# Kernel optimization log

Measured on AMD Instinct MI355X. Metric: run time of the kernel, lower is better.

The kernel has to match this reference:

```python
import jax, jax.numpy as jnp
import numpy as np
import math

IN_CH = 256
EMBED = 128


def setup_inputs() -> dict:
    key = jax.random.key(0)
    k1, k2, k3, k4, k5 = jax.random.split(key, 5)
    N, C, H, W = 4, IN_CH, 64, 64
    x = jax.random.normal(k1, (N, C, H, W), dtype=jnp.float32)
    # conv1x1 weights stored as [out_ch, in_ch] (kernel is 1x1)
    W_qkv = jax.random.normal(k2, (3 * EMBED, C), dtype=jnp.float32) * (1.0 / math.sqrt(C))
    b_qkv = jax.random.normal(k3, (3 * EMBED,), dtype=jnp.float32) * 0.01
    W_out = jax.random.normal(k4, (C, EMBED), dtype=jnp.float32) * (1.0 / math.sqrt(EMBED))
    b_out = jax.random.normal(k5, (C,), dtype=jnp.float32) * 0.01
    return {"x": x, "W_qkv": W_qkv, "b_qkv": b_qkv, "W_out": W_out, "b_out": b_out}


def reference(x, W_qkv, b_qkv, W_out, b_out):
    N, C, H, W = x.shape
    E = EMBED
    HW = H * W
    # conv1x1 QKV projection: (N, 3E, H, W)
    qkv = jnp.einsum('nchw,oc->nohw', x, W_qkv) + b_qkv[None, :, None, None]
    # faithful RAW C-order reshape (N, 3E, H, W) -> (N, HW, 3E), as in torch .reshape
    qkv = qkv.reshape(N, HW, 3 * E)
    q, k, v = jnp.split(qkv, 3, axis=-1)  # each (N, HW, E)
    # scores scaled by 1/sqrt(H*W), softmax over dim=-2 (columns)
    scores = jnp.einsum('nid,njd->nij', q, k) / math.sqrt(HW)
    soft = jax.nn.softmax(scores, axis=-2)
    out = jnp.einsum('nij,njd->nid', soft, v)  # (N, HW, E)
    # faithful RAW C-order reshape (N, HW, E) -> (N, E, H, W)
    out = out.reshape(N, E, H, W)
    # conv1x1 output projection
    y = jnp.einsum('nehw,ce->nchw', out, W_out) + b_out[None, :, None, None]
    return y
```

## Files before the change

kernel.cpp:

```cpp
#include <hip/hip_runtime.h>
#include <hip/hip_bf16.h>


typedef short bfrag __attribute__((ext_vector_type(8)));
typedef float ffrag __attribute__((ext_vector_type(4)));
typedef unsigned short us4 __attribute__((ext_vector_type(4)));
#define MFMA(a,b,c) __builtin_amdgcn_mfma_f32_16x16x32_bf16((a),(b),(c),0,0,0)

__device__ __forceinline__ unsigned short f2bf(float f){
  union { float f; unsigned u; } v; v.f = f;
  unsigned r = v.u + 0x7fffu + ((v.u >> 16) & 1u);
  return (unsigned short)(r >> 16);
}
__device__ __forceinline__ float bf2f(unsigned short h){
  union { unsigned u; float f; } v; v.u = ((unsigned)h) << 16; return v.f;
}
__device__ __forceinline__ unsigned bfpack(float a, float b){
  return (unsigned)f2bf(a) | ((unsigned)f2bf(b) << 16);
}

__global__ __launch_bounds__(256) void k_wcast(const float* __restrict__ Wq, const float* __restrict__ Wo,
                                               unsigned short* __restrict__ Wqb, unsigned short* __restrict__ Wob){
  int i = blockIdx.x*256 + threadIdx.x;
  if (i < 384*256) Wqb[i] = f2bf(Wq[i]);
  if (i < 256*128) Wob[i] = f2bf(Wo[i]);
}

__global__ __launch_bounds__(256) void k_qkv(const float* __restrict__ x, const unsigned short* __restrict__ Wqb,
                                             const float* __restrict__ bq, unsigned short* __restrict__ qkv){
  constexpr int LD = 136;
  __shared__ __align__(16) unsigned short As[128*LD];
  __shared__ __align__(16) unsigned short Bs[64*LD];
  const int o0 = blockIdx.x*128, h0 = blockIdx.y*64, n = blockIdx.z;
  const int t = threadIdx.x, w = t>>6, lane = t&63, lr = lane&15, q4 = lane>>4;
  ffrag acc[8] = {};
  for (int kh = 0; kh < 2; ++kh) {
    __syncthreads();
    #pragma unroll
    for (int r=0;r<8;++r){
      int pi = t + 256*r; int o = pi>>4, seg = pi&15;
      *(uint4*)&As[o*LD + seg*8] = *(const uint4*)(Wqb + (o0+o)*256 + kh*128 + seg*8);
    }
    #pragma unroll
    for (int r=0;r<8;++r){
      int idx = t + 256*r; int cl = idx>>4, h4 = idx&15;
      float4 v = *(const float4*)(x + (size_t)(n*256 + kh*128 + cl)*4096 + h0 + h4*4);
      Bs[(h4*4+0)*LD + cl] = f2bf(v.x);
      Bs[(h4*4+1)*LD + cl] = f2bf(v.y);
      Bs[(h4*4+2)*LD + cl] = f2bf(v.z);
      Bs[(h4*4+3)*LD + cl] = f2bf(v.w);
    }
    __syncthreads();
    #pragma unroll
    for (int kk=0;kk<4;++kk){
      bfrag a = *(const bfrag*)&Bs[(w*16+lr)*LD + kk*32 + q4*8];
      #pragma unroll
      for (int ot=0;ot<8;++ot){
        bfrag b = *(const bfrag*)&As[(ot*16+lr)*LD + kk*32 + q4*8];
        acc[ot] = MFMA(a,b,acc[ot]);
      }
    }
  }
  size_t base = (size_t)n*384*4096;
  #pragma unroll
  for (int ot=0;ot<8;++ot){
    int o  = o0 + ot*16 + lr;
    float bias = bq[o];
    int hw = h0 + w*16 + q4*4;
    us4 pk;
    pk.x = f2bf(acc[ot][0] + bias); pk.y = f2bf(acc[ot][1] + bias);
    pk.z = f2bf(acc[ot][2] + bias); pk.w = f2bf(acc[ot][3] + bias);
    *(us4*)(qkv + base + (size_t)o*4096 + hw) = pk;
  }
}

__global__ __launch_bounds__(256) void k_stats(const unsigned short* __restrict__ qkv,
                                               float* __restrict__ zp){
  constexpr int LD = 136;
  __shared__ __align__(16) unsigned short Qs[64*LD];
  const int j0 = blockIdx.x*256, ic = blockIdx.y, n = blockIdx.z;
  const int t = threadIdx.x, w = t>>6, lane = t&63, lr = lane&15, q4 = lane>>4;
  size_t base = (size_t)n*384*4096;
  bfrag kf[4][4];
  #pragma unroll
  for (int js=0; js<4; ++js){
    const unsigned short* krow = qkv + base + (size_t)(j0 + w*64 + js*16 + lr)*384 + 128;
    #pragma unroll
    for (int kk=0;kk<4;++kk) kf[js][kk] = *(const bfrag*)(krow + kk*32 + q4*8);
  }
  float Zc[16] = {};
  const float inv64 = 0.015625f;
  for (int rnd=0; rnd<8; ++rnd){
    int i0 = (ic<<9) + rnd*64;
    __syncthreads();
    #pragma unroll
    for (int r=0;r<4;++r){
      int pi = t + 256*r; int il = pi>>4, seg = pi&15;
      *(uint4*)&Qs[il*LD + seg*8] = *(const uint4*)(qkv + base + (size_t)(i0+il)*384 + seg*8);
    }
    __syncthreads();
    #pragma unroll
    for (int it=0; it<4; ++it){
      bfrag qb[4];
      #pragma unroll
      for (int kk=0;kk<4;++kk) qb[kk] = *(const bfrag*)&Qs[(it*16+lr)*LD + kk*32 + q4*8];
      #pragma unroll
      for (int js=0; js<4; ++js){
        ffrag s = {};
        #pragma unroll
        for (int kk=0;kk<4;++kk) s = MFMA(kf[js][kk], qb[kk], s);
        #pragma unroll
        for (int r=0;r<4;++r) Zc[js*4+r] += __expf(s[r]*inv64);
      }
    }
  }
  #pragma unroll
  for (int v=0; v<16; ++v){
    float z = Zc[v];
    z += __shfl_xor(z, 1); z += __shfl_xor(z, 2);
    z += __shfl_xor(z, 4); z += __shfl_xor(z, 8);
    Zc[v] = z;
  }
  if (lr == 0){
    int jb = j0 + w*64;
    float* zrow = zp + (size_t)((n<<3)+ic)*4096;
    #pragma unroll
    for (int js=0; js<4; ++js)
      #pragma unroll
      for (int r=0;r<4;++r)
        zrow[jb + js*16 + q4*4 + r] = Zc[js*4+r];
  }
}

__global__ __launch_bounds__(256) void k_vtrans(const unsigned short* __restrict__ qkv,
                                                const float* __restrict__ zp,
                                                unsigned short* __restrict__ vt,
                                                float* __restrict__ lse){
  constexpr int LD = 136;
  __shared__ __align__(16) unsigned short T[64*LD];
  const int p0 = blockIdx.x*64, n = blockIdx.y;
  const int t = threadIdx.x;
  size_t base = (size_t)n*384*4096;
  #pragma unroll
  for (int r=0;r<4;++r){
    int pi = t + 256*r; int pl = pi>>4, seg = pi&15;
    *(uint4*)&T[pl*LD + seg*8] = *(const uint4*)(qkv + base + (size_t)(p0+pl)*384 + 256 + seg*8);
  }
  if (t < 64){
    float Z = 0.f;
    #pragma unroll
    for (int c=0;c<8;++c) Z += zp[(size_t)((n<<3)+c)*4096 + p0 + t];
    lse[(n<<12) + p0 + t] = __logf(Z);
  }
  __syncthreads();
  unsigned* vt32 = (unsigned*)(vt + (size_t)n*128*4096);
  #pragma unroll
  for (int r=0;r<16;++r){
    int pi = t + 256*r;
    int d = pi>>5, k = pi&31;
    unsigned lo = T[(2*k)*LD + d];
    unsigned hi = T[(2*k+1)*LD + d];
    vt32[(size_t)d*2048 + (p0>>1) + k] = lo | (hi<<16);
  }
}

__global__ __launch_bounds__(256) void k_attn(const unsigned short* __restrict__ qkv,
                                              const unsigned short* __restrict__ vtg_all,
                                              const float* __restrict__ lse,
                                              unsigned short* __restrict__ part){
  constexpr int LDK = 136, LDV = 72, LDP = 72;
  __shared__ __align__(16) unsigned short Ks[64*LDK];
  __shared__ __align__(16) unsigned short Vt[128*LDV];
  __shared__ __align__(16) unsigned short Pw[4][32*LDP];
  __shared__ float Ls[64];
  const int i0 = blockIdx.x*128, jh = blockIdx.y, n = blockIdx.z;
  const int t = threadIdx.x, w = t>>6, lane = t&63, lr = lane&15, q4 = lane>>4;
  size_t base = (size_t)n*384*4096;
  const unsigned short* vtg = vtg_all + (size_t)n*128*4096;
  const float* lsen = lse + (n<<12);
  bfrag qf[2][4];
  #pragma unroll
  for (int isub=0;isub<2;++isub){
    const unsigned short* qrow = qkv + base + (size_t)(i0 + w*32 + isub*16 + lr)*384;
    #pragma unroll
    for (int kk=0;kk<4;++kk) qf[isub][kk] = *(const bfrag*)(qrow + kk*32 + q4*8);
  }
  ffrag acc[8][2] = {};
  const float inv64 = 0.015625f;
  for (int j0 = jh*1024; j0 < jh*1024+1024; j0 += 64){
    __syncthreads();
    #pragma unroll
    for (int r=0;r<4;++r){
      int pi = t + 256*r; int jl = pi>>4, seg = pi&15;
      *(uint4*)&Ks[jl*LDK + seg*8] = *(const uint4*)(qkv + base + (size_t)(j0+jl)*384 + 128 + seg*8);
    }
    #pragma unroll
    for (int r=0;r<4;++r){
      int pi = t + 256*r; int d = pi>>3, c = pi&7;
      *(uint4*)&Vt[d*LDV + c*8] = *(const uint4*)(vtg + (size_t)d*4096 + j0 + c*8);
    }
    if (t < 64) Ls[t] = lsen[j0 + t];
    __syncthreads();
    #pragma unroll
    for (int jt=0;jt<4;++jt){
      bfrag kf[4];
      #pragma unroll
      for (int kk=0;kk<4;++kk) kf[kk] = *(const bfrag*)&Ks[(jt*16+lr)*LDK + kk*32 + q4*8];
      float4 l4 = *(const float4*)&Ls[jt*16 + q4*4];
      #pragma unroll
      for (int isub=0;isub<2;++isub){
        ffrag s = {};
        #pragma unroll
        for (int kk=0;kk<4;++kk) s = MFMA(kf[kk], qf[isub][kk], s);
        float p0 = __expf(s[0]*inv64 - l4.x);
        float p1 = __expf(s[1]*inv64 - l4.y);
        float p2 = __expf(s[2]*inv64 - l4.z);
        float p3 = __expf(s[3]*inv64 - l4.w);
        uint2 pk; pk.x = bfpack(p0,p1); pk.y = bfpack(p2,p3);
        *(uint2*)&Pw[w][(isub*16+lr)*LDP + jt*16 + q4*4] = pk;
      }
    }
    asm volatile("" ::: "memory");
    #pragma unroll
    for (int jk=0;jk<2;++jk){
      bfrag pf0 = *(const bfrag*)&Pw[w][lr*LDP      + jk*32 + q4*8];
      bfrag pf1 = *(const bfrag*)&Pw[w][(16+lr)*LDP + jk*32 + q4*8];
      #pragma unroll
      for (int dt=0;dt<8;++dt){
        bfrag af = *(const bfrag*)&Vt[(dt*16+lr)*LDV + jk*32 + q4*8];
        acc[dt][0] = MFMA(af, pf0, acc[dt][0]);
        acc[dt][1] = MFMA(af, pf1, acc[dt][1]);
      }
    }
  }
  unsigned short* po = part + (size_t)(jh*4+n)*524288;
  #pragma unroll
  for (int isub=0;isub<2;++isub){
    const int i = i0 + w*32 + isub*16 + lr;
    #pragma unroll
    for (int dt=0;dt<8;++dt){
      us4 pk;
      pk.x = f2bf(acc[dt][isub][0]); pk.y = f2bf(acc[dt][isub][1]);
      pk.z = f2bf(acc[dt][isub][2]); pk.w = f2bf(acc[dt][isub][3]);
      *(us4*)(po + (size_t)i*128 + dt*16 + q4*4) = pk;
    }
  }
}

__global__ __launch_bounds__(256) void k_oproj(const unsigned short* __restrict__ part,
                                               const unsigned short* __restrict__ Wob,
                                               const float* __restrict__ bo, float* __restrict__ y){
  constexpr int LD = 136;
  __shared__ __align__(16) unsigned short As[128*LD];
  __shared__ __align__(16) unsigned short Rt[64*LD];
  const int c0 = blockIdx.x*128, h0 = blockIdx.y*64, n = blockIdx.z;
  const int t = threadIdx.x, w = t>>6, lane = t&63, lr = lane&15, q4 = lane>>4;
  #pragma unroll
  for (int r=0;r<8;++r){
    int pi = t + 256*r; int cl = pi>>4, seg = pi&15;
    *(uint4*)&As[cl*LD + seg*8] = *(const uint4*)(Wob + (c0+cl)*128 + seg*8);
  }
  #pragma unroll
  for (int r=0;r<4;++r){
    int pi = t + 256*r; int e = pi>>3, h8 = pi&7;
    size_t f = (size_t)e*4096 + h0 + h8*8;
    float a[8] = {};
    #pragma unroll
    for (int s=0;s<4;++s){
      uint4 u = *(const uint4*)(part + (size_t)(s*4+n)*524288 + f);
      a[0] += bf2f((unsigned short)(u.x & 0xffffu)); a[1] += bf2f((unsigned short)(u.x >> 16));
      a[2] += bf2f((unsigned short)(u.y & 0xffffu)); a[3] += bf2f((unsigned short)(u.y >> 16));
      a[4] += bf2f((unsigned short)(u.z & 0xffffu)); a[5] += bf2f((unsigned short)(u.z >> 16));
      a[6] += bf2f((unsigned short)(u.w & 0xffffu)); a[7] += bf2f((unsigned short)(u.w >> 16));
    }
    #pragma unroll
    for (int k=0;k<8;++k) Rt[(h8*8+k)*LD + e] = f2bf(a[k]);
  }
  __syncthreads();
  ffrag acc[8] = {};
  #pragma unroll
  for (int kk=0;kk<4;++kk){
    bfrag a = *(const bfrag*)&Rt[(w*16+lr)*LD + kk*32 + q4*8];
    #pragma unroll
    for (int cs=0;cs<8;++cs){
      bfrag b = *(const bfrag*)&As[(cs*16+lr)*LD + kk*32 + q4*8];
      acc[cs] = MFMA(a,b,acc[cs]);
    }
  }
  #pragma unroll
  for (int cs=0;cs<8;++cs){
    int c = c0 + cs*16 + lr;
    float bias = bo[c];
    float4 v4 = { acc[cs][0]+bias, acc[cs][1]+bias, acc[cs][2]+bias, acc[cs][3]+bias };
    *(float4*)(y + ((size_t)n*256 + c)*4096 + h0 + w*16 + q4*4) = v4;
  }
}

extern "C" void kernel_launch(void* const* d_in, const int* in_sizes, int n_in,
                              void* d_out, int out_size, void* d_ws, size_t ws_size,
                              hipStream_t stream){
  const float* x  = (const float*)d_in[0];
  const float* Wq = (const float*)d_in[1];
  const float* bq = (const float*)d_in[2];
  const float* Wo = (const float*)d_in[3];
  const float* bo = (const float*)d_in[4];
  float* y = (float*)d_out;
  char* ws = (char*)d_ws;
  unsigned short* qkv  = (unsigned short*)(ws + 0);
  unsigned short* vtg  = (unsigned short*)(ws + 12582912);
  unsigned short* Wqb  = (unsigned short*)(ws + 16777216);
  unsigned short* Wob  = (unsigned short*)(ws + 16973824);
  float* zp   = (float*)(ws + 17039360);
  float* lse  = (float*)(ws + 17563648);
  unsigned short* part = (unsigned short*)(ws + 17629184);

  k_wcast <<<dim3(384),     256, 0, stream>>>(Wq, Wo, Wqb, Wob);
  k_qkv   <<<dim3(3,64,4),  256, 0, stream>>>(x, Wqb, bq, qkv);
  k_stats <<<dim3(16,8,4),  256, 0, stream>>>(qkv, zp);
  k_vtrans<<<dim3(64,4),    256, 0, stream>>>(qkv, zp, vtg, lse);
  k_attn  <<<dim3(32,4,4),  256, 0, stream>>>(qkv, vtg, lse, part);
  k_oproj <<<dim3(2,64,4),  256, 0, stream>>>(part, Wob, bo, y);
}
```

Before: 181.5 us.

## Fuse weight casts into GEMMs, widen QKV tile, swizzle P buffer, split attention keys further

Drops the separate weight-cast kernel: the QKV and output-projection kernels now convert the fp32 weights to bf16 while staging them into LDS. The QKV kernel computes all 384 output channels per block, so each x tile is loaded and converted once, at the cost of much more LDS and 24 accumulators per thread. The attention kernel's P scratch buffer uses an XOR-swizzled layout in place of padding, to avoid LDS bank conflicts. When the workspace is large enough, the key range is split into 8 slices instead of 4, giving more blocks in exchange for more partial-sum traffic in the output projection.

Result: slower. 203.1 us (+11.9%).

```diff
diff --git a/kernel.cpp b/kernel.cpp
--- a/kernel.cpp
+++ b/kernel.cpp
@@ -18,28 +18,26 @@
 __device__ __forceinline__ unsigned bfpack(float a, float b){
   return (unsigned)f2bf(a) | ((unsigned)f2bf(b) << 16);
 }
-
-__global__ __launch_bounds__(256) void k_wcast(const float* __restrict__ Wq, const float* __restrict__ Wo,
-                                               unsigned short* __restrict__ Wqb, unsigned short* __restrict__ Wob){
-  int i = blockIdx.x*256 + threadIdx.x;
-  if (i < 384*256) Wqb[i] = f2bf(Wq[i]);
-  if (i < 256*128) Wob[i] = f2bf(Wo[i]);
-}
-
-__global__ __launch_bounds__(256) void k_qkv(const float* __restrict__ x, const unsigned short* __restrict__ Wqb,
+__device__ __forceinline__ uint4 pack8(float4 a, float4 b){
+  uint4 u; u.x = bfpack(a.x,a.y); u.y = bfpack(a.z,a.w);
+  u.z = bfpack(b.x,b.y); u.w = bfpack(b.z,b.w); return u;
+}
+
+__global__ __launch_bounds__(256) void k_qkv(const float* __restrict__ x, const float* __restrict__ Wq,
                                              const float* __restrict__ bq, unsigned short* __restrict__ qkv){
   constexpr int LD = 136;
-  __shared__ __align__(16) unsigned short As[128*LD];
+  __shared__ __align__(16) unsigned short As[384*LD];
   __shared__ __align__(16) unsigned short Bs[64*LD];
-  const int o0 = blockIdx.x*128, h0 = blockIdx.y*64, n = blockIdx.z;
+  const int h0 = blockIdx.x*64, n = blockIdx.y;
   const int t = threadIdx.x, w = t>>6, lane = t&63, lr = lane&15, q4 = lane>>4;
-  ffrag acc[8] = {};
+  ffrag acc[24] = {};
   for (int kh = 0; kh < 2; ++kh) {
     __syncthreads();
     #pragma unroll
-    for (int r=0;r<8;++r){
+    for (int r=0;r<24;++r){
       int pi = t + 256*r; int o = pi>>4, seg = pi&15;
-      *(uint4*)&As[o*LD + seg*8] = *(const uint4*)(Wqb + (o0+o)*256 + kh*128 + seg*8);
+      const float* wp = Wq + (size_t)o*256 + kh*128 + seg*8;
+      *(uint4*)&As[o*LD + seg*8] = pack8(*(const float4*)wp, *(const float4*)(wp+4));
     }
     #pragma unroll
     for (int r=0;r<8;++r){
@@ -55,7 +53,7 @@
     for (int kk=0;kk<4;++kk){
       bfrag a = *(const bfrag*)&Bs[(w*16+lr)*LD + kk*32 + q4*8];
       #pragma unroll
-      for (int ot=0;ot<8;++ot){
+      for (int ot=0;ot<24;++ot){
         bfrag b = *(const bfrag*)&As[(ot*16+lr)*LD + kk*32 + q4*8];
         acc[ot] = MFMA(a,b,acc[ot]);
       }
@@ -63,8 +61,8 @@
   }
   size_t base = (size_t)n*384*4096;
   #pragma unroll
-  for (int ot=0;ot<8;++ot){
-    int o  = o0 + ot*16 + lr;
+  for (int ot=0;ot<24;++ot){
+    int o  = ot*16 + lr;
     float bias = bq[o];
     int hw = h0 + w*16 + q4*4;
     us4 pk;
@@ -164,14 +162,15 @@
   }
 }
 
+template<int JSPAN>
 __global__ __launch_bounds__(256) void k_attn(const unsigned short* __restrict__ qkv,
                                               const unsigned short* __restrict__ vtg_all,
                                               const float* __restrict__ lse,
                                               unsigned short* __restrict__ part){
-  constexpr int LDK = 136, LDV = 72, LDP = 72;
+  constexpr int LDK = 136, LDV = 72;
   __shared__ __align__(16) unsigned short Ks[64*LDK];
   __shared__ __align__(16) unsigned short Vt[128*LDV];
-  __shared__ __align__(16) unsigned short Pw[4][32*LDP];
+  __shared__ __align__(16) unsigned short Pw[4][32*64];
   __shared__ float Ls[64];
   const int i0 = blockIdx.x*128, jh = blockIdx.y, n = blockIdx.z;
   const int t = threadIdx.x, w = t>>6, lane = t&63, lr = lane&15, q4 = lane>>4;
@@ -187,7 +186,8 @@
   }
   ffrag acc[8][2] = {};
   const float inv64 = 0.015625f;
-  for (int j0 = jh*1024; j0 < jh*1024+1024; j0 += 64){
+  const int sw = (lr & 7);
+  for (int j0 = jh*JSPAN; j0 < jh*JSPAN+JSPAN; j0 += 64){
     __syncthreads();
     #pragma unroll
     for (int r=0;r<4;++r){
@@ -217,14 +217,16 @@
         float p2 = __expf(s[2]*inv64 - l4.z);
         float p3 = __expf(s[3]*inv64 - l4.w);
         uint2 pk; pk.x = bfpack(p0,p1); pk.y = bfpack(p2,p3);
-        *(uint2*)&Pw[w][(isub*16+lr)*LDP + jt*16 + q4*4] = pk;
+        int c8s = ((jt*2 + (q4>>1)) ^ sw);
+        *(uint2*)&Pw[w][(isub*16+lr)*64 + c8s*8 + (q4&1)*4] = pk;
       }
     }
     asm volatile("" ::: "memory");
     #pragma unroll
     for (int jk=0;jk<2;++jk){
-      bfrag pf0 = *(const bfrag*)&Pw[w][lr*LDP      + jk*32 + q4*8];
-      bfrag pf1 = *(const bfrag*)&Pw[w][(16+lr)*LDP + jk*32 + q4*8];
+      int c8s = ((jk*4 + q4) ^ sw);
+      bfrag pf0 = *(const bfrag*)&Pw[w][lr*64      + c8s*8];
+      bfrag pf1 = *(const bfrag*)&Pw[w][(16+lr)*64 + c8s*8];
       #pragma unroll
       for (int dt=0;dt<8;++dt){
         bfrag af = *(const bfrag*)&Vt[(dt*16+lr)*LDV + jk*32 + q4*8];
@@ -247,8 +249,9 @@
   }
 }
 
+template<int NSL>
 __global__ __launch_bounds__(256) void k_oproj(const unsigned short* __restrict__ part,
-                                               const unsigned short* __restrict__ Wob,
+                                               const float* __restrict__ Wo,
                                                const float* __restrict__ bo, float* __restrict__ y){
   constexpr int LD = 136;
   __shared__ __align__(16) unsigned short As[128*LD];
@@ -258,7 +261,8 @@
   #pragma unroll
   for (int r=0;r<8;++r){
     int pi = t + 256*r; int cl = pi>>4, seg = pi&15;
-    *(uint4*)&As[cl*LD + seg*8] = *(const uint4*)(Wob + (c0+cl)*128 + seg*8);
+    const float* wp = Wo + (size_t)(c0+cl)*128 + seg*8;
+    *(uint4*)&As[cl*LD + seg*8] = pack8(*(const float4*)wp, *(const float4*)(wp+4));
   }
   #pragma unroll
   for (int r=0;r<4;++r){
@@ -266,7 +270,7 @@
     size_t f = (size_t)e*4096 + h0 + h8*8;
     float a[8] = {};
     #pragma unroll
-    for (int s=0;s<4;++s){
+    for (int s=0;s<NSL;++s){
       uint4 u = *(const uint4*)(part + (size_t)(s*4+n)*524288 + f);
       a[0] += bf2f((unsigned short)(u.x & 0xffffu)); a[1] += bf2f((unsigned short)(u.x >> 16));
       a[2] += bf2f((unsigned short)(u.y & 0xffffu)); a[3] += bf2f((unsigned short)(u.y >> 16));
@@ -308,16 +312,20 @@
   char* ws = (char*)d_ws;
   unsigned short* qkv  = (unsigned short*)(ws + 0);
   unsigned short* vtg  = (unsigned short*)(ws + 12582912);
-  unsigned short* Wqb  = (unsigned short*)(ws + 16777216);
-  unsigned short* Wob  = (unsigned short*)(ws + 16973824);
-  float* zp   = (float*)(ws + 17039360);
-  float* lse  = (float*)(ws + 17563648);
-  unsigned short* part = (unsigned short*)(ws + 17629184);
-
-  k_wcast <<<dim3(384),     256, 0, stream>>>(Wq, Wo, Wqb, Wob);
-  k_qkv   <<<dim3(3,64,4),  256, 0, stream>>>(x, Wqb, bq, qkv);
+  float* zp   = (float*)(ws + 16777216);
+  float* lse  = (float*)(ws + 17301504);
+  unsigned short* part = (unsigned short*)(ws + 17367040);
+
+  const bool big = ws_size >= (size_t)17367040 + (size_t)32*1048576;
+
+  k_qkv   <<<dim3(64,4),    256, 0, stream>>>(x, Wq, bq, qkv);
   k_stats <<<dim3(16,8,4),  256, 0, stream>>>(qkv, zp);
   k_vtrans<<<dim3(64,4),    256, 0, stream>>>(qkv, zp, vtg, lse);
-  k_attn  <<<dim3(32,4,4),  256, 0, stream>>>(qkv, vtg, lse, part);
-  k_oproj <<<dim3(2,64,4),  256, 0, stream>>>(part, Wob, bo, y);
-}
+  if (big){
+    k_attn<512> <<<dim3(32,8,4), 256, 0, stream>>>(qkv, vtg, lse, part);
+    k_oproj<8>  <<<dim3(2,64,4), 256, 0, stream>>>(part, Wo, bo, y);
+  } else {
+    k_attn<1024><<<dim3(32,4,4), 256, 0, stream>>>(qkv, vtg, lse, part);
+    k_oproj<4>  <<<dim3(2,64,4), 256, 0, stream>>>(part, Wo, bo, y);
+  }
+}
```
